# Kernel optimization log

Measured on AMD Instinct MI355X. Metric: run time of the kernel, lower is better.

## Reference

```python
import jax, jax.numpy as jnp
import numpy as np

EPS = 1e-5

def conv2d(x, w, b=None, pad=1):
    # x: [B,C,H,W], w: [O,I,kh,kw]
    y = jax.lax.conv_general_dilated(x, w, (1, 1), [(pad, pad), (pad, pad)],
                                     dimension_numbers=('NCHW', 'OIHW', 'NCHW'))
    if b is not None:
        y = y + b[None, :, None, None]
    return y

def bn(x, g, b, m, v):
    # inference-mode batchnorm
    inv = g / jnp.sqrt(v + EPS)
    return x * inv[None, :, None, None] + (b - m * inv)[None, :, None, None]

def coord_conv(x, w, b):
    B, C, H, W = x.shape
    yy = jnp.broadcast_to(jnp.linspace(-1.0, 1.0, H)[:, None], (H, W))
    xx = jnp.broadcast_to(jnp.linspace(-1.0, 1.0, W)[None, :], (H, W))
    coords = jnp.broadcast_to(jnp.stack([xx, yy])[None], (B, 2, H, W)).astype(x.dtype)
    return conv2d(jnp.concatenate([x, coords], axis=1), w, b, pad=1)

def deform_conv(x, offset, w):
    # deformable conv v1, 3x3, pad=1, stride=1, no bias
    B, C, H, W = x.shape
    K = 9
    # offset channels interleaved (y, x) per kernel tap
    off = offset.reshape(B, K, 2, H, W)
    off_y, off_x = off[:, :, 0], off[:, :, 1]          # [B,9,H,W]
    k = jnp.arange(K)
    ko_y = (k // 3 - 1).astype(x.dtype)[None, :, None, None]
    ko_x = (k % 3 - 1).astype(x.dtype)[None, :, None, None]
    base_y = jnp.arange(H, dtype=x.dtype)[None, None, :, None]
    base_x = jnp.arange(W, dtype=x.dtype)[None, None, None, :]
    py = base_y + ko_y + off_y                          # [B,9,H,W]
    px = base_x + ko_x + off_x
    xf = x.reshape(B, C, H * W)
    y0 = jnp.floor(py)
    x0 = jnp.floor(px)
    acc = jnp.zeros((B, C, K, H, W), x.dtype)
    for dy in (0.0, 1.0):
        for dx in (0.0, 1.0):
            yy = y0 + dy
            xx = x0 + dx
            wgt = (1.0 - jnp.abs(py - yy)) * (1.0 - jnp.abs(px - xx))
            valid = (yy >= 0) & (yy < H) & (xx >= 0) & (xx < W)
            wgt = jnp.where(valid, wgt, 0.0)            # zero padding OOB
            yi = jnp.clip(yy, 0, H - 1).astype(jnp.int32)
            xi = jnp.clip(xx, 0, W - 1).astype(jnp.int32)
            idx = (yi * W + xi).reshape(B, K * H * W)
            v = jnp.take_along_axis(xf, idx[:, None, :], axis=2).reshape(B, C, K, H, W)
            acc = acc + v * wgt[:, None]
    wk = w.reshape(w.shape[0], w.shape[1], K)           # [O,I,9]
    return jnp.einsum('bckhw,ock->bohw', acc, wk)

def setup_inputs() -> dict:
    key = jax.random.key(0)
    ks = jax.random.split(key, 16)
    d_model, hd = 256, 64
    B, H, W = 8, 96, 96
    f32 = jnp.float32
    def bn_params(k):
        k1, k2, k3 = jax.random.split(k, 3)
        return (1.0 + 0.1 * jax.random.normal(k1, (hd,), f32),
                0.1 * jax.random.normal(k2, (hd,), f32),
                0.1 * jax.random.normal(k3, (hd,), f32),
                0.5 + jax.random.uniform(jax.random.fold_in(k, 7), (hd,), f32))
    bn1 = bn_params(ks[1]); bn2 = bn_params(ks[2]); bn3 = bn_params(ks[3]); bn4 = bn_params(ks[4])
    inp = {
        'features': jax.random.normal(ks[0], (B, H, W, d_model), f32),
        'coord_w': 0.05 * jax.random.normal(ks[5], (hd, d_model + 2, 3, 3), f32),
        'coord_b': jnp.zeros((hd,), f32),
        'bn1_g': bn1[0], 'bn1_b': bn1[1], 'bn1_m': bn1[2], 'bn1_v': bn1[3],
        'off_w': 0.01 * jax.random.normal(ks[6], (18, hd, 3, 3), f32),
        'off_b': 0.01 * jax.random.normal(ks[7], (18,), f32),
        'dc_w': 0.05 * jax.random.normal(ks[8], (hd, hd, 3, 3), f32),
        'bn2_g': bn2[0], 'bn2_b': bn2[1], 'bn2_m': bn2[2], 'bn2_v': bn2[3],
        'r1_w': 0.05 * jax.random.normal(ks[9], (hd, hd, 3, 3), f32),
        'bn3_g': bn3[0], 'bn3_b': bn3[1], 'bn3_m': bn3[2], 'bn3_v': bn3[3],
        'r2_w': 0.05 * jax.random.normal(ks[10], (hd, hd, 3, 3), f32),
        'bn4_g': bn4[0], 'bn4_b': bn4[1], 'bn4_m': bn4[2], 'bn4_v': bn4[3],
        'out_w': 0.1 * jax.random.normal(ks[11], (1, hd, 1, 1), f32),
        'out_b': jnp.zeros((1,), f32),
    }
    return inp

def reference(features, coord_w, coord_b, bn1_g, bn1_b, bn1_m, bn1_v,
              off_w, off_b, dc_w, bn2_g, bn2_b, bn2_m, bn2_v,
              r1_w, bn3_g, bn3_b, bn3_m, bn3_v,
              r2_w, bn4_g, bn4_b, bn4_m, bn4_v, out_w, out_b):
    x = jnp.transpose(features, (0, 3, 1, 2))           # NHWC -> NCHW
    x = jax.nn.relu(bn(coord_conv(x, coord_w, coord_b), bn1_g, bn1_b, bn1_m, bn1_v))
    offset = conv2d(x, off_w, off_b, pad=1)
    x = deform_conv(x, offset, dc_w)
    x = jax.nn.relu(bn(x, bn2_g, bn2_b, bn2_m, bn2_v))
    x = jax.nn.relu(bn(conv2d(x, r1_w, None, pad=1), bn3_g, bn3_b, bn3_m, bn3_v))
    x = jax.nn.relu(bn(conv2d(x, r2_w, None, pad=1), bn4_g, bn4_b, bn4_m, bn4_v))
    return jax.nn.sigmoid(conv2d(x, out_w, out_b, pad=0))
```

## Files before the change

### kernel.cpp

```cpp
#include <hip/hip_runtime.h>


typedef unsigned short u16;
typedef unsigned int u32;
typedef __attribute__((ext_vector_type(8)))  short bf16x8;
typedef __attribute__((ext_vector_type(16))) float f32x16;

#define EPSBN 1e-5f

__device__ __forceinline__ u16 f2bf(float f) {
  u32 u = __builtin_bit_cast(u32, f);
  u32 r = u + 0x7FFFu + ((u >> 16) & 1u);
  return (u16)(r >> 16);
}
__device__ __forceinline__ u32 pk2(float a, float b) {
  return (u32)f2bf(a) | ((u32)f2bf(b) << 16);
}
__device__ __forceinline__ float lo2f(u32 w) { return __builtin_bit_cast(float, w << 16); }
__device__ __forceinline__ float hi2f(u32 w) { return __builtin_bit_cast(float, w & 0xFFFF0000u); }

#define N_WCF 147456
#define N_WCC 9216
#define N_WOF 18432
#define N_W64 36864
#define N_ALLW (N_WCF + N_WCC + N_WOF + 3*N_W64)

__global__ __launch_bounds__(256) void prep_kernel(
    const float* __restrict__ coord_w, const float* __restrict__ off_w,
    const float* __restrict__ dc_w, const float* __restrict__ r1_w,
    const float* __restrict__ r2_w,
    u16* __restrict__ wcf, u16* __restrict__ wcc, u16* __restrict__ wof,
    u16* __restrict__ wdf, u16* __restrict__ wr1, u16* __restrict__ wr2)
{
  int i = blockIdx.x * 256 + threadIdx.x;
  if (i >= N_ALLW) return;
  int d = i;
  if (d < N_WCF) {
    int j = d & 7, lane = (d >> 3) & 63, frag = d >> 9;
    int nt = frag & 1, h = (frag >> 1) & 3, tap = (frag >> 3) % 9, cc = (frag >> 3) / 9;
    int ic = cc * 64 + h * 16 + ((lane >> 5) << 3) + j;
    int oc = nt * 32 + (lane & 31);
    wcf[d] = f2bf(coord_w[((size_t)oc * 258 + ic) * 9 + tap]);
    return;
  }
  d -= N_WCF;
  if (d < N_WCC) {
    int j = d & 7, lane = (d >> 3) & 63, frag = d >> 9;
    int nt = frag & 1, tap = frag >> 1;
    int ic = 256 + ((lane >> 5) << 3) + j;
    int oc = nt * 32 + (lane & 31);
    wcc[d] = (ic < 258) ? f2bf(coord_w[((size_t)oc * 258 + ic) * 9 + tap]) : (u16)0;
    return;
  }
  d -= N_WCC;
  if (d < N_WOF) {
    int j = d & 7, lane = (d >> 3) & 63, frag = d >> 9;
    int h = frag & 3, tap = frag >> 2;
    int ic = h * 16 + ((lane >> 5) << 3) + j;
    int oc = lane & 31;
    wof[d] = (oc < 18) ? f2bf(off_w[((size_t)oc * 64 + ic) * 9 + tap]) : (u16)0;
    return;
  }
  d -= N_WOF;
  int seg = d / N_W64;
  int e = d - seg * N_W64;
  int j = e & 7, lane = (e >> 3) & 63, frag = e >> 9;
  int nt = frag & 1, h = (frag >> 1) & 3, tap = frag >> 3;
  int ic = h * 16 + ((lane >> 5) << 3) + j;
  int oc = nt * 32 + (lane & 31);
  const float* src = (seg == 0) ? dc_w : (seg == 1) ? r1_w : r2_w;
  u16* dst = (seg == 0) ? wdf : (seg == 1) ? wr1 : wr2;
  dst[e] = f2bf(src[((size_t)oc * 64 + ic) * 9 + tap]);
}

__global__ __launch_bounds__(512, 4) void coord_conv_kernel(
    const float* __restrict__ feat, const u16* __restrict__ wcf,
    const u16* __restrict__ wcc, const float* __restrict__ cb,
    const float* __restrict__ g, const float* __restrict__ bb,
    const float* __restrict__ m, const float* __restrict__ v,
    u16* __restrict__ x1b)
{
  __shared__ __align__(16) u16 tile[6 * 34 * 72];
  const int t = threadIdx.x;
  const int wv = t >> 6, lane = t & 63;
  const int l31 = lane & 31, l5 = lane >> 5;
  const int row = wv & 3, ntw = wv >> 2;
  const int x0 = blockIdx.x * 32, y0 = blockIdx.y * 4, b = blockIdx.z;

  f32x16 acc = {};
  float4 pa[4], pb[4];

  auto issue = [&](int cc) {
    #pragma unroll
    for (int r = 0; r < 4; ++r) {
      const int i = t + r * 512;
      const float4 z = {0.f, 0.f, 0.f, 0.f};
      pa[r] = z; pb[r] = z;
      if (i < 1632) {
        const int px = i >> 3, gg = i & 7;
        const int ly = px / 34, lx = px - ly * 34;
        const int gy = y0 + ly - 1, gx = x0 + lx - 1;
        if ((unsigned)gy < 96u && (unsigned)gx < 96u) {
          const float* p = feat + ((size_t)((b * 96 + gy) * 96 + gx)) * 256
                           + cc * 64 + gg * 8;
          pa[r] = *(const float4*)p;
          pb[r] = *(const float4*)(p + 4);
        }
      }
    }
  };
  auto commit = [&]() {
    #pragma unroll
    for (int r = 0; r < 4; ++r) {
      const int i = t + r * 512;
      if (i < 1632) {
        const int px = i >> 3, gg = i & 7;
        uint4 o;
        o.x = pk2(pa[r].x, pa[r].y); o.y = pk2(pa[r].z, pa[r].w);
        o.z = pk2(pb[r].x, pb[r].y); o.w = pk2(pb[r].z, pb[r].w);
        *(uint4*)(tile + px * 72 + gg * 8) = o;
      }
    }
  };

  issue(0);
  for (int cc = 0; cc < 4; ++cc) {
    __syncthreads();
    commit();
    __syncthreads();
    if (cc < 3) issue(cc + 1);
    #pragma unroll
    for (int tap = 0; tap < 9; ++tap) {
      const int dy = tap / 3, dx = tap - dy * 3;
      #pragma unroll
      for (int h = 0; h < 4; ++h) {
        const bf16x8 afr = *(const bf16x8*)(tile +
            ((row + dy) * 34 + l31 + dx) * 72 + h * 16 + l5 * 8);
        const bf16x8 bfr = *(const bf16x8*)(wcf +
            ((size_t)((((cc * 9 + tap) * 4 + h) * 2) + ntw)) * 512 + lane * 8);
        acc = __builtin_amdgcn_mfma_f32_32x32x16_bf16(afr, bfr, acc, 0, 0, 0);
      }
    }
  }

  __syncthreads();
  for (int i = t; i < 408; i += 512) {
    const int px = i >> 1, gg = i & 1;
    const int ly = px / 34, lx = px - ly * 34;
    const int gy = y0 + ly - 1, gx = x0 + lx - 1;
    uint4 o = {0u, 0u, 0u, 0u};
    if (gg == 0 && (unsigned)gy < 96u && (unsigned)gx < 96u) {
      const float xx = -1.f + (2.f / 95.f) * (float)gx;
      const float yy = -1.f + (2.f / 95.f) * (float)gy;
      o.x = pk2(xx, yy);
    }
    *(uint4*)(tile + (ly * 34 + lx) * 72 + gg * 8) = o;
  }
  __syncthreads();
  #pragma unroll
  for (int tap = 0; tap < 9; ++tap) {
    const int dy = tap / 3, dx = tap - dy * 3;
    const bf16x8 afr = *(const bf16x8*)(tile +
        ((row + dy) * 34 + l31 + dx) * 72 + l5 * 8);
    const bf16x8 bfr = *(const bf16x8*)(wcc +
        ((size_t)(tap * 2 + ntw)) * 512 + lane * 8);
    acc = __builtin_amdgcn_mfma_f32_32x32x16_bf16(afr, bfr, acc, 0, 0, 0);
  }

  const int y = y0 + row;
  const int oc = ntw * 32 + l31;
  const float inv = g[oc] * rsqrtf(v[oc] + EPSBN);
  const float sh = bb[oc] - m[oc] * inv + cb[oc] * inv;
  #pragma unroll
  for (int r = 0; r < 16; ++r) {
    const int xr = (r & 3) + 8 * (r >> 2) + 4 * l5;
    const float val = fmaxf(fmaf(acc[r], inv, sh), 0.f);
    x1b[((size_t)((b * 96 + y) * 96 + x0 + xr)) * 64 + oc] = f2bf(val);
  }
}

template<int NN, int EPI>
__global__ __launch_bounds__(512, 4) void conv64_kernel(
    const u16* __restrict__ xin, const u16* __restrict__ wf,
    const float* __restrict__ bias,
    const float* __restrict__ g, const float* __restrict__ bb,
    const float* __restrict__ m, const float* __restrict__ v,
    const float* __restrict__ ow, const float* __restrict__ ob,
    void* __restrict__ outp)
{
  __shared__ __align__(16) u16 tile[6 * 34 * 72];
  __shared__ float red[2][128];
  const int t = threadIdx.x;
  const int wv = t >> 6, lane = t & 63;
  const int l31 = lane & 31, l5 = lane >> 5;
  const int row = wv & 3, ntw = wv >> 2;
  const int x0 = blockIdx.x * 32, y0 = blockIdx.y * 4, b = blockIdx.z;

  uint4 pf[4];
  #pragma unroll
  for (int r = 0; r < 4; ++r) {
    const int i = t + r * 512;
    const uint4 z = {0u, 0u, 0u, 0u};
    pf[r] = z;
    if (i < 1632) {
      const int px = i >> 3, gg = i & 7;
      const int ly = px / 34, lx = px - ly * 34;
      const int gy = y0 + ly - 1, gx = x0 + lx - 1;
      if ((unsigned)gy < 96u && (unsigned)gx < 96u)
        pf[r] = *(const uint4*)(xin + (((size_t)((b * 96 + gy) * 96 + gx)) << 6)
                                + gg * 8);
    }
  }
  #pragma unroll
  for (int r = 0; r < 4; ++r) {
    const int i = t + r * 512;
    if (i < 1632) {
      const int px = i >> 3, gg = i & 7;
      *(uint4*)(tile + px * 72 + gg * 8) = pf[r];
    }
  }
  __syncthreads();

  f32x16 acc = {};
  #pragma unroll
  for (int tap = 0; tap < 9; ++tap) {
    const int dy = tap / 3, dx = tap - dy * 3;
    if constexpr (NN == 2) {
      #pragma unroll
      for (int h = 0; h < 4; ++h) {
        const bf16x8 afr = *(const bf16x8*)(tile +
            ((row + dy) * 34 + l31 + dx) * 72 + h * 16 + l5 * 8);
        const bf16x8 bfr = *(const bf16x8*)(wf +
            ((size_t)((tap * 4 + h) * 2 + ntw)) * 512 + lane * 8);
        acc = __builtin_amdgcn_mfma_f32_32x32x16_bf16(afr, bfr, acc, 0, 0, 0);
      }
    } else {
      #pragma unroll
      for (int hh = 0; hh < 2; ++hh) {
        const int h = ntw * 2 + hh;
        const bf16x8 afr = *(const bf16x8*)(tile +
            ((row + dy) * 34 + l31 + dx) * 72 + h * 16 + l5 * 8);
        const bf16x8 bfr = *(const bf16x8*)(wf +
            ((size_t)(tap * 4 + h)) * 512 + lane * 8);
        acc = __builtin_amdgcn_mfma_f32_32x32x16_bf16(afr, bfr, acc, 0, 0, 0);
      }
    }
  }

  const int y = y0 + row;
  if constexpr (EPI == 0) {
    u16* xo = (u16*)outp;
    const int oc = ntw * 32 + l31;
    const float inv = g[oc] * rsqrtf(v[oc] + EPSBN);
    const float sh = bb[oc] - m[oc] * inv;
    #pragma unroll
    for (int r = 0; r < 16; ++r) {
      const int xr = (r & 3) + 8 * (r >> 2) + 4 * l5;
      const float val = fmaxf(fmaf(acc[r], inv, sh), 0.f);
      xo[((size_t)((b * 96 + y) * 96 + x0 + xr)) * 64 + oc] = f2bf(val);
    }
  } else if constexpr (EPI == 1) {
    __syncthreads();
    float* redk = (float*)tile;
    if (ntw == 1) {
      #pragma unroll
      for (int r = 0; r < 16; ++r)
        redk[r * 256 + row * 64 + lane] = acc[r];
    }
    __syncthreads();
    if (ntw == 0) {
      #pragma unroll
      for (int r = 0; r < 16; ++r)
        acc[r] += redk[r * 256 + row * 64 + lane];
      float* fo = (float*)outp;
      const int oc = l31;
      if (oc < 18) {
        const float bs = bias[oc];
        #pragma unroll
        for (int r = 0; r < 16; ++r) {
          const int xr = (r & 3) + 8 * (r >> 2) + 4 * l5;
          fo[((size_t)((b * 96 + y) * 96 + x0 + xr)) * 18 + oc] = acc[r] + bs;
        }
      }
    }
  } else {
    float pr[16];
    #pragma unroll
    for (int r = 0; r < 16; ++r) pr[r] = 0.f;
    {
      const int oc = ntw * 32 + l31;
      const float inv = g[oc] * rsqrtf(v[oc] + EPSBN);
      const float sh = bb[oc] - m[oc] * inv;
      const float wo = ow[oc];
      #pragma unroll
      for (int r = 0; r < 16; ++r) {
        const float val = fmaxf(fmaf(acc[r], inv, sh), 0.f);
        pr[r] = fmaf(val, wo, pr[r]);
      }
    }
    #pragma unroll
    for (int mask = 1; mask <= 16; mask <<= 1)
      #pragma unroll
      for (int r = 0; r < 16; ++r)
        pr[r] += __shfl_xor(pr[r], mask);
    if (l31 == 0) {
      #pragma unroll
      for (int r = 0; r < 16; ++r) {
        const int xr = (r & 3) + 8 * (r >> 2) + 4 * l5;
        red[ntw][row * 32 + xr] = pr[r];
      }
    }
    __syncthreads();
    if (t < 128) {
      float* fo = (float*)outp;
      const int yy = y0 + (t >> 5), xx = x0 + (t & 31);
      const float val = red[0][t] + red[1][t] + ob[0];
      fo[(size_t)(b * 96 + yy) * 96 + xx] = 1.f / (1.f + expf(-val));
    }
  }
}

__global__ __launch_bounds__(512, 4) void deform_kernel(
    const u16* __restrict__ x1b, const float* __restrict__ off,
    const u16* __restrict__ wdf,
    const float* __restrict__ g, const float* __restrict__ bb,
    const float* __restrict__ m, const float* __restrict__ v,
    u16* __restrict__ x2b)
{
  __shared__ __align__(16) u16 s[2 * 128 * 72];
  __shared__ float offs[128 * 18];
  const int t = threadIdx.x;
  const int wv = t >> 6, lane = t & 63;
  const int l31 = lane & 31, l5 = lane >> 5;
  const int mt = wv & 3, ntw = wv >> 2;
  const int x0 = blockIdx.x * 16, y0 = blockIdx.y * 8, b = blockIdx.z;

  {
    float po[5];
    #pragma unroll
    for (int r = 0; r < 5; ++r) {
      const int i = t + r * 512;
      po[r] = 0.f;
      if (i < 2304) {
        const int p = i / 18, c = i - p * 18;
        const int gy = y0 + (p >> 4), gx = x0 + (p & 15);
        po[r] = off[((size_t)((b * 96 + gy) * 96 + gx)) * 18 + c];
      }
    }
    #pragma unroll
    for (int r = 0; r < 5; ++r) {
      const int i = t + r * 512;
      if (i < 2304) offs[i] = po[r];
    }
  }
  __syncthreads();

  const int sp = t >> 2, part = t & 3;
  const int sy = y0 + (sp >> 4), sx = x0 + (sp & 15);

  uint4 gbuf[8];
  float w4[4];

  auto prefetch = [&](int k) {
    const float oy = offs[sp * 18 + 2 * k];
    const float ox = offs[sp * 18 + 2 * k + 1];
    const float py = (float)(sy + k / 3 - 1) + oy;
    const float px = (float)(sx + k % 3 - 1) + ox;
    const float yf = floorf(py), xf = floorf(px);
    const float fy = py - yf, fx = px - xf;
    const int yi = (int)yf, xi = (int)xf;
    #pragma unroll
    for (int cor = 0; cor < 4; ++cor) {
      const int cy = yi + (cor >> 1), cx = xi + (cor & 1);
      const uint4 z = {0u, 0u, 0u, 0u};
      gbuf[2 * cor] = z; gbuf[2 * cor + 1] = z;
      const float wy = (cor & 2) ? fy : 1.f - fy;
      const float wx = (cor & 1) ? fx : 1.f - fx;
      w4[cor] = 0.f;
      if ((unsigned)cy < 96u && (unsigned)cx < 96u) {
        w4[cor] = wy * wx;
        const u16* p = x1b + ((size_t)((b * 96 + cy) * 96 + cx)) * 64
                       + part * 16;
        gbuf[2 * cor]     = *(const uint4*)p;
        gbuf[2 * cor + 1] = *(const uint4*)(p + 8);
      }
    }
  };
  auto combine = [&](u16* dst) {
    float val[16];
    #pragma unroll
    for (int j = 0; j < 16; ++j) val[j] = 0.f;
    #pragma unroll
    for (int cor = 0; cor < 4; ++cor) {
      const float wgt = w4[cor];
      const u32 uu[8] = {gbuf[2 * cor].x, gbuf[2 * cor].y,
                         gbuf[2 * cor].z, gbuf[2 * cor].w,
                         gbuf[2 * cor + 1].x, gbuf[2 * cor + 1].y,
                         gbuf[2 * cor + 1].z, gbuf[2 * cor + 1].w};
      #pragma unroll
      for (int u = 0; u < 8; ++u) {
        val[2 * u]     = fmaf(wgt, lo2f(uu[u]), val[2 * u]);
        val[2 * u + 1] = fmaf(wgt, hi2f(uu[u]), val[2 * u + 1]);
      }
    }
    u32 pk[8];
    #pragma unroll
    for (int u = 0; u < 8; ++u) pk[u] = pk2(val[2 * u], val[2 * u + 1]);
    uint4 w0 = {pk[0], pk[1], pk[2], pk[3]};
    uint4 w1 = {pk[4], pk[5], pk[6], pk[7]};
    *(uint4*)(dst + sp * 72 + part * 16) = w0;
    *(uint4*)(dst + sp * 72 + part * 16 + 8) = w1;
  };

  f32x16 acc = {};

  prefetch(0);
  combine(s);
  __syncthreads();

  for (int k = 0; k < 9; ++k) {
    u16* cur = s + (k & 1) * 9216;
    if (k < 8) prefetch(k + 1);
    #pragma unroll
    for (int h = 0; h < 4; ++h) {
      const bf16x8 afr = *(const bf16x8*)(cur + (mt * 32 + l31) * 72
                                          + h * 16 + l5 * 8);
      const bf16x8 bfr = *(const bf16x8*)(wdf +
          ((size_t)((k * 4 + h) * 2 + ntw)) * 512 + lane * 8);
      acc = __builtin_amdgcn_mfma_f32_32x32x16_bf16(afr, bfr, acc, 0, 0, 0);
    }
    if (k < 8) combine(s + ((k + 1) & 1) * 9216);
    __syncthreads();
  }

  const int oc = ntw * 32 + l31;
  const float inv = g[oc] * rsqrtf(v[oc] + EPSBN);
  const float sh = bb[oc] - m[oc] * inv;
  #pragma unroll
  for (int r = 0; r < 16; ++r) {
    const int pxi = mt * 32 + (r & 3) + 8 * (r >> 2) + 4 * l5;
    const int y = y0 + (pxi >> 4), x = x0 + (pxi & 15);
    const float val = fmaxf(fmaf(acc[r], inv, sh), 0.f);
    x2b[((size_t)((b * 96 + y) * 96 + x)) * 64 + oc] = f2bf(val);
  }
}

extern "C" void kernel_launch(void* const* d_in, const int* in_sizes, int n_in,
                              void* d_out, int out_size, void* d_ws,
                              size_t ws_size, hipStream_t stream)
{
  (void)in_sizes; (void)n_in; (void)out_size; (void)ws_size;
  const float* features = (const float*)d_in[0];
  const float* coord_w  = (const float*)d_in[1];
  const float* coord_b  = (const float*)d_in[2];
  const float* bn1g = (const float*)d_in[3];
  const float* bn1b = (const float*)d_in[4];
  const float* bn1m = (const float*)d_in[5];
  const float* bn1v = (const float*)d_in[6];
  const float* off_w = (const float*)d_in[7];
  const float* off_b = (const float*)d_in[8];
  const float* dc_w  = (const float*)d_in[9];
  const float* bn2g = (const float*)d_in[10];
  const float* bn2b = (const float*)d_in[11];
  const float* bn2m = (const float*)d_in[12];
  const float* bn2v = (const float*)d_in[13];
  const float* r1_w = (const float*)d_in[14];
  const float* bn3g = (const float*)d_in[15];
  const float* bn3b = (const float*)d_in[16];
  const float* bn3m = (const float*)d_in[17];
  const float* bn3v = (const float*)d_in[18];
  const float* r2_w = (const float*)d_in[19];
  const float* bn4g = (const float*)d_in[20];
  const float* bn4b = (const float*)d_in[21];
  const float* bn4m = (const float*)d_in[22];
  const float* bn4v = (const float*)d_in[23];
  const float* out_w = (const float*)d_in[24];
  const float* out_b = (const float*)d_in[25];

  char* W = (char*)d_ws;
  float* offb = (float*)W;
  u16*   x1b  = (u16*)(W + 5308416);
  u16*   x2b  = (u16*)(W + 14745600);
  u16*   x3b  = (u16*)(W + 24182784);
  u16*   wcf  = (u16*)(W + 33619968);
  u16*   wcc  = wcf + N_WCF;
  u16*   wof  = wcc + N_WCC;
  u16*   wdf  = wof + N_WOF;
  u16*   wr1  = wdf + N_W64;
  u16*   wr2  = wr1 + N_W64;

  prep_kernel<<<(N_ALLW + 255) / 256, 256, 0, stream>>>(
      coord_w, off_w, dc_w, r1_w, r2_w, wcf, wcc, wof, wdf, wr1, wr2);

  dim3 grid(3, 24, 8);
  dim3 gridD(6, 12, 8);

  coord_conv_kernel<<<grid, 512, 0, stream>>>(
      features, wcf, wcc, coord_b, bn1g, bn1b, bn1m, bn1v, x1b);
  conv64_kernel<1, 1><<<grid, 512, 0, stream>>>(
      x1b, wof, off_b, nullptr, nullptr, nullptr, nullptr, nullptr, nullptr,
      (void*)offb);
  deform_kernel<<<gridD, 512, 0, stream>>>(
      x1b, offb, wdf, bn2g, bn2b, bn2m, bn2v, x2b);
  conv64_kernel<2, 0><<<grid, 512, 0, stream>>>(
      x2b, wr1, nullptr, bn3g, bn3b, bn3m, bn3v, nullptr, nullptr, (void*)x3b);
  conv64_kernel<2, 2><<<grid, 512, 0, stream>>>(
      x3b, wr2, nullptr, bn4g, bn4b, bn4m, bn4v, out_w, out_b, d_out);
}
```

Measured before the change: 252.6 us.

## Split K across wave halves and keep weight fragments in registers for convs

The coord conv and conv64 kernels now assign each wave two output rows and half of the input-channel range. Each wave preloads its weight fragments into registers once instead of reloading them from global memory for every MFMA, and reuses each B fragment across two rows. The two K-halves are then summed through shared memory before the epilogue. This is meant to cut global weight traffic and raise MFMA operand reuse. In exchange it adds more registers, with launch bounds lowered from 4 to 2 blocks per SM, plus extra syncs for the reduction.

```diff
diff --git a/kernel.cpp b/kernel.cpp
--- a/kernel.cpp
+++ b/kernel.cpp
@@ -73,7 +73,7 @@
   dst[e] = f2bf(src[((size_t)oc * 64 + ic) * 9 + tap]);
 }
 
-__global__ __launch_bounds__(512, 4) void coord_conv_kernel(
+__global__ __launch_bounds__(512, 2) void coord_conv_kernel(
     const float* __restrict__ feat, const u16* __restrict__ wcf,
     const u16* __restrict__ wcc, const float* __restrict__ cb,
     const float* __restrict__ g, const float* __restrict__ bb,
@@ -84,13 +84,14 @@
   const int t = threadIdx.x;
   const int wv = t >> 6, lane = t & 63;
   const int l31 = lane & 31, l5 = lane >> 5;
-  const int row = wv & 3, ntw = wv >> 2;
+  const int rp = wv & 1, ntw = (wv >> 1) & 1, kh = wv >> 2;
   const int x0 = blockIdx.x * 32, y0 = blockIdx.y * 4, b = blockIdx.z;
 
-  f32x16 acc = {};
+  f32x16 acc[2] = {};
   float4 pa[4], pb[4];
-
-  auto issue = [&](int cc) {
+  bf16x8 wfr[18];
+
+  auto issueF = [&](int cc) {
     #pragma unroll
     for (int r = 0; r < 4; ++r) {
       const int i = t + r * 512;
@@ -109,7 +110,7 @@
       }
     }
   };
-  auto commit = [&]() {
+  auto commitF = [&]() {
     #pragma unroll
     for (int r = 0; r < 4; ++r) {
       const int i = t + r * 512;
@@ -122,27 +123,50 @@
       }
     }
   };
-
-  issue(0);
+  auto loadW = [&](int cc) {
+    #pragma unroll
+    for (int tap = 0; tap < 9; ++tap)
+      #pragma unroll
+      for (int hh = 0; hh < 2; ++hh) {
+        const int h = kh * 2 + hh;
+        wfr[tap * 2 + hh] = *(const bf16x8*)(wcf +
+            ((size_t)((((cc * 9 + tap) * 4 + h) * 2) + ntw)) * 512 + lane * 8);
+      }
+  };
+
+  issueF(0);
+  loadW(0);
   for (int cc = 0; cc < 4; ++cc) {
     __syncthreads();
-    commit();
-    __syncthreads();
-    if (cc < 3) issue(cc + 1);
+    commitF();
+    __syncthreads();
+    if (cc < 3) issueF(cc + 1);
     #pragma unroll
     for (int tap = 0; tap < 9; ++tap) {
       const int dy = tap / 3, dx = tap - dy * 3;
       #pragma unroll
-      for (int h = 0; h < 4; ++h) {
-        const bf16x8 afr = *(const bf16x8*)(tile +
-            ((row + dy) * 34 + l31 + dx) * 72 + h * 16 + l5 * 8);
-        const bf16x8 bfr = *(const bf16x8*)(wcf +
-            ((size_t)((((cc * 9 + tap) * 4 + h) * 2) + ntw)) * 512 + lane * 8);
-        acc = __builtin_amdgcn_mfma_f32_32x32x16_bf16(afr, bfr, acc, 0, 0, 0);
-      }
-    }
-  }
-
+      for (int hh = 0; hh < 2; ++hh) {
+        const bf16x8 bfr = wfr[tap * 2 + hh];
+        #pragma unroll
+        for (int ai = 0; ai < 2; ++ai) {
+          const bf16x8 afr = *(const bf16x8*)(tile +
+              ((rp * 2 + ai + dy) * 34 + l31 + dx) * 72
+              + (kh * 2 + hh) * 16 + l5 * 8);
+          acc[ai] = __builtin_amdgcn_mfma_f32_32x32x16_bf16(afr, bfr, acc[ai],
+                                                            0, 0, 0);
+        }
+      }
+    }
+    if (cc < 3) loadW(cc + 1);
+  }
+
+  bf16x8 wcr[9];
+  if (kh == 0) {
+    #pragma unroll
+    for (int tap = 0; tap < 9; ++tap)
+      wcr[tap] = *(const bf16x8*)(wcc + ((size_t)(tap * 2 + ntw)) * 512
+                                  + lane * 8);
+  }
   __syncthreads();
   for (int i = t; i < 408; i += 512) {
     const int px = i >> 1, gg = i & 1;
@@ -157,30 +181,57 @@
     *(uint4*)(tile + (ly * 34 + lx) * 72 + gg * 8) = o;
   }
   __syncthreads();
-  #pragma unroll
-  for (int tap = 0; tap < 9; ++tap) {
-    const int dy = tap / 3, dx = tap - dy * 3;
-    const bf16x8 afr = *(const bf16x8*)(tile +
-        ((row + dy) * 34 + l31 + dx) * 72 + l5 * 8);
-    const bf16x8 bfr = *(const bf16x8*)(wcc +
-        ((size_t)(tap * 2 + ntw)) * 512 + lane * 8);
-    acc = __builtin_amdgcn_mfma_f32_32x32x16_bf16(afr, bfr, acc, 0, 0, 0);
-  }
-
-  const int y = y0 + row;
-  const int oc = ntw * 32 + l31;
-  const float inv = g[oc] * rsqrtf(v[oc] + EPSBN);
-  const float sh = bb[oc] - m[oc] * inv + cb[oc] * inv;
-  #pragma unroll
-  for (int r = 0; r < 16; ++r) {
-    const int xr = (r & 3) + 8 * (r >> 2) + 4 * l5;
-    const float val = fmaxf(fmaf(acc[r], inv, sh), 0.f);
-    x1b[((size_t)((b * 96 + y) * 96 + x0 + xr)) * 64 + oc] = f2bf(val);
+  if (kh == 0) {
+    #pragma unroll
+    for (int tap = 0; tap < 9; ++tap) {
+      const int dy = tap / 3, dx = tap - dy * 3;
+      #pragma unroll
+      for (int ai = 0; ai < 2; ++ai) {
+        const bf16x8 afr = *(const bf16x8*)(tile +
+            ((rp * 2 + ai + dy) * 34 + l31 + dx) * 72 + l5 * 8);
+        acc[ai] = __builtin_amdgcn_mfma_f32_32x32x16_bf16(afr, wcr[tap],
+                                                          acc[ai], 0, 0, 0);
+      }
+    }
+  }
+
+  float* redk = (float*)tile;
+  const int slot = wv & 3;
+  #pragma unroll
+  for (int ai = 0; ai < 2; ++ai) {
+    __syncthreads();
+    if (kh == 1) {
+      #pragma unroll
+      for (int r = 0; r < 16; ++r)
+        redk[(r * 4 + slot) * 64 + lane] = acc[ai][r];
+    }
+    __syncthreads();
+    if (kh == 0) {
+      #pragma unroll
+      for (int r = 0; r < 16; ++r)
+        acc[ai][r] += redk[(r * 4 + slot) * 64 + lane];
+    }
+  }
+
+  if (kh == 0) {
+    const int oc = ntw * 32 + l31;
+    const float inv = g[oc] * rsqrtf(v[oc] + EPSBN);
+    const float sh = bb[oc] - m[oc] * inv + cb[oc] * inv;
+    #pragma unroll
+    for (int ai = 0; ai < 2; ++ai) {
+      const int y = y0 + rp * 2 + ai;
+      #pragma unroll
+      for (int r = 0; r < 16; ++r) {
+        const int xr = (r & 3) + 8 * (r >> 2) + 4 * l5;
+        const float val = fmaxf(fmaf(acc[ai][r], inv, sh), 0.f);
+        x1b[((size_t)((b * 96 + y) * 96 + x0 + xr)) * 64 + oc] = f2bf(val);
+      }
+    }
   }
 }
 
 template<int NN, int EPI>
-__global__ __launch_bounds__(512, 4) void conv64_kernel(
+__global__ __launch_bounds__(512, 2) void conv64_kernel(
     const u16* __restrict__ xin, const u16* __restrict__ wf,
     const float* __restrict__ bias,
     const float* __restrict__ g, const float* __restrict__ bb,
@@ -189,11 +240,14 @@
     void* __restrict__ outp)
 {
   __shared__ __align__(16) u16 tile[6 * 34 * 72];
-  __shared__ float red[2][128];
+  __shared__ float red2[2][128];
   const int t = threadIdx.x;
   const int wv = t >> 6, lane = t & 63;
   const int l31 = lane & 31, l5 = lane >> 5;
-  const int row = wv & 3, ntw = wv >> 2;
+  const int rp  = (NN == 2) ? (wv & 1) : 0;
+  const int ntw = (NN == 2) ? ((wv >> 1) & 1) : 0;
+  const int row = (NN == 2) ? 0 : (wv & 3);
+  const int kh  = wv >> 2;
   const int x0 = blockIdx.x * 32, y0 = blockIdx.y * 4, b = blockIdx.z;
 
   uint4 pf[4];
@@ -211,6 +265,16 @@
                                 + gg * 8);
     }
   }
+  bf16x8 wfr[18];
+  #pragma unroll
+  for (int tap = 0; tap < 9; ++tap)
+    #pragma unroll
+    for (int hh = 0; hh < 2; ++hh) {
+      const int h = kh * 2 + hh;
+      const size_t f = (NN == 2) ? (size_t)((tap * 4 + h) * 2 + ntw)
+                                 : (size_t)(tap * 4 + h);
+      wfr[tap * 2 + hh] = *(const bf16x8*)(wf + f * 512 + lane * 8);
+    }
   #pragma unroll
   for (int r = 0; r < 4; ++r) {
     const int i = t + r * 512;
@@ -221,100 +285,104 @@
   }
   __syncthreads();
 
-  f32x16 acc = {};
+  constexpr int NA = (NN == 2) ? 2 : 1;
+  f32x16 acc[NA] = {};
   #pragma unroll
   for (int tap = 0; tap < 9; ++tap) {
     const int dy = tap / 3, dx = tap - dy * 3;
-    if constexpr (NN == 2) {
-      #pragma unroll
-      for (int h = 0; h < 4; ++h) {
+    #pragma unroll
+    for (int hh = 0; hh < 2; ++hh) {
+      const int h = kh * 2 + hh;
+      #pragma unroll
+      for (int ai = 0; ai < NA; ++ai) {
+        const int rr = (NN == 2) ? (rp * 2 + ai) : row;
         const bf16x8 afr = *(const bf16x8*)(tile +
-            ((row + dy) * 34 + l31 + dx) * 72 + h * 16 + l5 * 8);
-        const bf16x8 bfr = *(const bf16x8*)(wf +
-            ((size_t)((tap * 4 + h) * 2 + ntw)) * 512 + lane * 8);
-        acc = __builtin_amdgcn_mfma_f32_32x32x16_bf16(afr, bfr, acc, 0, 0, 0);
-      }
-    } else {
-      #pragma unroll
-      for (int hh = 0; hh < 2; ++hh) {
-        const int h = ntw * 2 + hh;
-        const bf16x8 afr = *(const bf16x8*)(tile +
-            ((row + dy) * 34 + l31 + dx) * 72 + h * 16 + l5 * 8);
-        const bf16x8 bfr = *(const bf16x8*)(wf +
-            ((size_t)(tap * 4 + h)) * 512 + lane * 8);
-        acc = __builtin_amdgcn_mfma_f32_32x32x16_bf16(afr, bfr, acc, 0, 0, 0);
-      }
-    }
-  }
-
-  const int y = y0 + row;
+            ((rr + dy) * 34 + l31 + dx) * 72 + h * 16 + l5 * 8);
+        acc[ai] = __builtin_amdgcn_mfma_f32_32x32x16_bf16(afr, wfr[tap * 2 + hh],
+                                                          acc[ai], 0, 0, 0);
+      }
+    }
+  }
+
+  float* redk = (float*)tile;
+  const int slot = (NN == 2) ? (wv & 3) : row;
+  #pragma unroll
+  for (int ai = 0; ai < NA; ++ai) {
+    __syncthreads();
+    if (kh == 1) {
+      #pragma unroll
+      for (int r = 0; r < 16; ++r)
+        redk[(r * 4 + slot) * 64 + lane] = acc[ai][r];
+    }
+    __syncthreads();
+    if (kh == 0) {
+      #pragma unroll
+      for (int r = 0; r < 16; ++r)
+        acc[ai][r] += redk[(r * 4 + slot) * 64 + lane];
+    }
+  }
+
   if constexpr (EPI == 0) {
-    u16* xo = (u16*)outp;
-    const int oc = ntw * 32 + l31;
-    const float inv = g[oc] * rsqrtf(v[oc] + EPSBN);
-    const float sh = bb[oc] - m[oc] * inv;
-    #pragma unroll
-    for (int r = 0; r < 16; ++r) {
-      const int xr = (r & 3) + 8 * (r >> 2) + 4 * l5;
-      const float val = fmaxf(fmaf(acc[r], inv, sh), 0.f);
-      xo[((size_t)((b * 96 + y) * 96 + x0 + xr)) * 64 + oc] = f2bf(val);
-    }
-  } else if constexpr (EPI == 1) {
-    __syncthreads();
-    float* redk = (float*)tile;
-    if (ntw == 1) {
-      #pragma unroll
-      for (int r = 0; r < 16; ++r)
-        redk[r * 256 + row * 64 + lane] = acc[r];
-    }
-    __syncthreads();
-    if (ntw == 0) {
-      #pragma unroll
-      for (int r = 0; r < 16; ++r)
-        acc[r] += redk[r * 256 + row * 64 + lane];
-      float* fo = (float*)outp;
-      const int oc = l31;
-      if (oc < 18) {
-        const float bs = bias[oc];
+    if (kh == 0) {
+      u16* xo = (u16*)outp;
+      const int oc = ntw * 32 + l31;
+      const float inv = g[oc] * rsqrtf(v[oc] + EPSBN);
+      const float sh = bb[oc] - m[oc] * inv;
+      #pragma unroll
+      for (int ai = 0; ai < NA; ++ai) {
+        const int y = y0 + rp * 2 + ai;
         #pragma unroll
         for (int r = 0; r < 16; ++r) {
           const int xr = (r & 3) + 8 * (r >> 2) + 4 * l5;
-          fo[((size_t)((b * 96 + y) * 96 + x0 + xr)) * 18 + oc] = acc[r] + bs;
+          const float val = fmaxf(fmaf(acc[ai][r], inv, sh), 0.f);
+          xo[((size_t)((b * 96 + y) * 96 + x0 + xr)) * 64 + oc] = f2bf(val);
         }
       }
     }
+  } else if constexpr (EPI == 1) {
+    if (kh == 0 && l31 < 18) {
+      float* fo = (float*)outp;
+      const int y = y0 + row;
+      const float bs = bias[l31];
+      #pragma unroll
+      for (int r = 0; r < 16; ++r) {
+        const int xr = (r & 3) + 8 * (r >> 2) + 4 * l5;
+        fo[((size_t)((b * 96 + y) * 96 + x0 + xr)) * 18 + l31] = acc[0][r] + bs;
+      }
+    }
   } else {
-    float pr[16];
-    #pragma unroll
-    for (int r = 0; r < 16; ++r) pr[r] = 0.f;
-    {
+    if (kh == 0) {
       const int oc = ntw * 32 + l31;
       const float inv = g[oc] * rsqrtf(v[oc] + EPSBN);
       const float sh = bb[oc] - m[oc] * inv;
       const float wo = ow[oc];
       #pragma unroll
-      for (int r = 0; r < 16; ++r) {
-        const float val = fmaxf(fmaf(acc[r], inv, sh), 0.f);
-        pr[r] = fmaf(val, wo, pr[r]);
-      }
-    }
-    #pragma unroll
-    for (int mask = 1; mask <= 16; mask <<= 1)
-      #pragma unroll
-      for (int r = 0; r < 16; ++r)
-        pr[r] += __shfl_xor(pr[r], mask);
-    if (l31 == 0) {
-      #pragma unroll
-      for (int r = 0; r < 16; ++r) {
-        const int xr = (r & 3) + 8 * (r >> 2) + 4 * l5;
-        red[ntw][row * 32 + xr] = pr[r];
+      for (int ai = 0; ai < NA; ++ai) {
+        float pr[16];
+        #pragma unroll
+        for (int r = 0; r < 16; ++r) {
+          const float val = fmaxf(fmaf(acc[ai][r], inv, sh), 0.f);
+          pr[r] = val * wo;
+        }
+        #pragma unroll
+        for (int mask = 1; mask <= 16; mask <<= 1)
+          #pragma unroll
+          for (int r = 0; r < 16; ++r)
+            pr[r] += __shfl_xor(pr[r], mask);
+        if (l31 == 0) {
+          #pragma unroll
+          for (int r = 0; r < 16; ++r) {
+            const int xr = (r & 3) + 8 * (r >> 2) + 4 * l5;
+            red2[ntw][(rp * 2 + ai) * 32 + xr] = pr[r];
+          }
+        }
       }
     }
     __syncthreads();
     if (t < 128) {
       float* fo = (float*)outp;
       const int yy = y0 + (t >> 5), xx = x0 + (t & 31);
-      const float val = red[0][t] + red[1][t] + ob[0];
+      const float val = red2[0][t] + red2[1][t] + ob[0];
       fo[(size_t)(b * 96 + yy) * 96 + xx] = 1.f / (1.f + expf(-val));
     }
   }
```

Measured after the change: 251.0 us, median of 2. Within noise of the previous version (-0.7%).
